# Optimization experiments

Hardware: AMD Instinct MI355X
Metric: run time of the kernel (lower is better)

Reference implementation:

```python
import jax, jax.numpy as jnp
from jax import lax
import numpy as np

RADIUS = 0.2
NSAMPLE = 32


def setup_inputs() -> dict:
    key = jax.random.key(0)
    ks = jax.random.split(key, 6)
    B, N, C = 4, 16384, 64
    xyz = jax.random.uniform(ks[0], (B, N, 3), dtype=jnp.float32)
    points = jax.random.normal(ks[1], (B, N, C), dtype=jnp.float32)
    w1 = jax.random.normal(ks[2], (64, C + 3), dtype=jnp.float32) * 0.05
    b1 = jnp.zeros((64,), jnp.float32)
    w2 = jax.random.normal(ks[3], (128, 64), dtype=jnp.float32) * 0.05
    b2 = jnp.zeros((128,), jnp.float32)
    return {"xyz": xyz, "points": points, "w1": w1, "b1": b1, "w2": w2, "b2": b2, "npoint": 1024}


def farthest_point_sampling(xyz, npoint):
    # xyz: (B,N,3). Deterministic start at index 0 (original uses a random start).
    B, N, _ = xyz.shape
    bidx = jnp.arange(B)

    def step(carry, _):
        distance, farthest = carry
        centroid = xyz[bidx, farthest]  # (B,3)
        dist = jnp.sum((xyz - centroid[:, None, :]) ** 2, axis=-1)  # (B,N)
        distance = jnp.minimum(distance, dist)
        nxt = jnp.argmax(distance, axis=-1)
        return (distance, nxt), farthest

    init = (jnp.full((B, N), 1e10, xyz.dtype), jnp.zeros((B,), jnp.int32))
    _, cents = lax.scan(step, init, None, length=npoint)  # (npoint,B)
    return cents.T  # (B,npoint)


def ball_query(xyz, new_xyz, radius, nsample):
    # xyz:(B,N,3) new_xyz:(B,S,3) -> (B,S,nsample) int indices
    N = xyz.shape[1]
    sqrdists = jnp.sum((new_xyz[:, :, None, :] - xyz[:, None, :, :]) ** 2, axis=-1)  # (B,S,N)
    idx = jnp.where(sqrdists > radius ** 2, N, jnp.arange(N))
    idx = jnp.sort(idx, axis=-1)[:, :, :nsample]
    first = idx[:, :, :1]
    return jnp.where(idx == N, first, idx)


def index_points(points, idx):
    # points:(B,N,C) idx:(B,...) -> (B,...,C)
    return jax.vmap(lambda p, i: p[i])(points, idx)


def reference(xyz, points, w1, b1, w2, b2, npoint):
    centroids = farthest_point_sampling(xyz, npoint)  # (B,S)
    new_xyz = index_points(xyz, centroids)  # (B,S,3)
    group_idx = ball_query(xyz, new_xyz, RADIUS, NSAMPLE)  # (B,S,K)
    grouped_xyz = index_points(xyz, group_idx)  # (B,S,K,3)
    grouped_xyz_norm = grouped_xyz - new_xyz[:, :, None, :]
    grouped_points = index_points(points, group_idx)  # (B,S,K,C)
    feats = jnp.concatenate([grouped_xyz_norm, grouped_points], axis=-1)  # (B,S,K,C+3)
    h = jax.nn.relu(jnp.einsum('bskc,oc->bsko', feats, w1) + b1)
    h = jax.nn.relu(jnp.einsum('bskc,oc->bsko', h, w2) + b2)  # (B,S,K,out)
    new_points = jnp.max(h, axis=2)  # (B,S,out)
    return (new_xyz, new_points)
```

## Files before the change

kernel.cpp:

```cpp
#include <hip/hip_runtime.h>

#define BB 4
#define NN 16384
#define CC 64
#define NPOINT 1024
#define NSAMPLE 32

#define FPS_T 1024
#define NCHUNK 256
#define NCELL 4096

#define REPEAT16(M) M(0) M(1) M(2) M(3) M(4) M(5) M(6) M(7) \
                    M(8) M(9) M(10) M(11) M(12) M(13) M(14) M(15)

__global__ __launch_bounds__(FPS_T) void fps_kernel(const float* __restrict__ xyz,
                                                    float* __restrict__ new_xyz,
                                                    float4* __restrict__ sorted) {
    #pragma clang fp contract(off)
    extern __shared__ char smem_raw[];
    float2* sxy  = (float2*)smem_raw;
    int*    hist = (int*)(smem_raw + 131072);
    float*  outc = (float*)(smem_raw + 131072);
    float*  lox  = (float*)(smem_raw + 147456);
    float*  loy  = lox + 272;
    float*  loz  = loy + 272;
    float*  hix  = loz + 272;
    float*  hiy  = hix + 272;
    float*  hiz  = hiy + 272;
    float4* wbc  = (float4*)(smem_raw + 153984);
    unsigned long long* slot = (unsigned long long*)(smem_raw + 154496);
    int*    wsum = (int*)(smem_raw + 154528);

    const int b    = blockIdx.x;
    const int tid  = threadIdx.x;
    const int lane = tid & 63;
    const int wv   = tid >> 6;
    const float* bx = xyz + (size_t)b * NN * 3;
    float4* sb = sorted + (size_t)b * NN;

    #pragma unroll
    for (int j = 0; j < 4; ++j) hist[j * FPS_T + tid] = 0;
    __syncthreads();

    #pragma unroll
    for (int j = 0; j < 16; ++j) {
        const int p = j * FPS_T + tid;
        const float x = bx[p * 3 + 0], y = bx[p * 3 + 1], z = bx[p * 3 + 2];
        int cx = (int)(x * 16.0f); cx = cx > 15 ? 15 : (cx < 0 ? 0 : cx);
        int cy = (int)(y * 16.0f); cy = cy > 15 ? 15 : (cy < 0 ? 0 : cy);
        int cz = (int)(z * 16.0f); cz = cz > 15 ? 15 : (cz < 0 ? 0 : cz);
        int code = 0;
        #pragma unroll
        for (int i = 0; i < 4; ++i)
            code |= (((cx >> i) & 1) << (3 * i)) |
                    (((cy >> i) & 1) << (3 * i + 1)) |
                    (((cz >> i) & 1) << (3 * i + 2));
        atomicAdd(&hist[code], 1);
    }
    __syncthreads();

    {
        const int h0 = hist[4 * tid + 0], h1 = hist[4 * tid + 1];
        const int h2 = hist[4 * tid + 2], h3 = hist[4 * tid + 3];
        const int s  = h0 + h1 + h2 + h3;
        int v = s;
        #pragma unroll
        for (int o = 1; o < 64; o <<= 1) {
            const int u = __shfl_up(v, o, 64);
            if (lane >= o) v += u;
        }
        if (lane == 63) wsum[wv] = v;
        __syncthreads();
        int base = 0;
        for (int w = 0; w < wv; ++w) base += wsum[w];
        const int e0 = base + v - s;
        hist[4 * tid + 0] = e0;
        hist[4 * tid + 1] = e0 + h0;
        hist[4 * tid + 2] = e0 + h0 + h1;
        hist[4 * tid + 3] = e0 + h0 + h1 + h2;
    }
    __syncthreads();

    #pragma unroll
    for (int j = 0; j < 16; ++j) {
        const int p = j * FPS_T + tid;
        const float x = bx[p * 3 + 0], y = bx[p * 3 + 1], z = bx[p * 3 + 2];
        int cx = (int)(x * 16.0f); cx = cx > 15 ? 15 : (cx < 0 ? 0 : cx);
        int cy = (int)(y * 16.0f); cy = cy > 15 ? 15 : (cy < 0 ? 0 : cy);
        int cz = (int)(z * 16.0f); cz = cz > 15 ? 15 : (cz < 0 ? 0 : cz);
        int code = 0;
        #pragma unroll
        for (int i = 0; i < 4; ++i)
            code |= (((cx >> i) & 1) << (3 * i)) |
                    (((cy >> i) & 1) << (3 * i + 1)) |
                    (((cz >> i) & 1) << (3 * i + 2));
        const int slotg = atomicAdd(&hist[code], 1);
        sb[slotg]  = make_float4(x, y, z, __int_as_float(p));
        sxy[slotg] = make_float2(x, y);
    }
    __syncthreads();

#define DECLZ(k) float z##k; unsigned long long key##k;
    REPEAT16(DECLZ)
#undef DECLZ
    float abx0 = 0.f, aby0 = 0.f, abz0 = 0.f, abx1 = 0.f, aby1 = 0.f, abz1 = 0.f;

#define AABBPRE(k) { const int g = wv + ((k) << 4);                       \
    const float4 pt = sb[(g << 6) + lane];                                \
    z##k = pt.z;                                                          \
    key##k = (((unsigned long long)__float_as_uint(1e10f)) << 32) |       \
             ((unsigned long long)(0x3FFFu -                              \
                    (unsigned)__float_as_int(pt.w)) << 4);                \
    float mnx = pt.x, mxx = pt.x, mny = pt.y, mxy = pt.y,                 \
          mnz = pt.z, mxz = pt.z;                                         \
    _Pragma("unroll")                                                     \
    for (int m = 32; m >= 1; m >>= 1) {                                   \
        mnx = fminf(mnx, __shfl_xor(mnx, m, 64));                         \
        mxx = fmaxf(mxx, __shfl_xor(mxx, m, 64));                         \
        mny = fminf(mny, __shfl_xor(mny, m, 64));                         \
        mxy = fmaxf(mxy, __shfl_xor(mxy, m, 64));                         \
        mnz = fminf(mnz, __shfl_xor(mnz, m, 64));                         \
        mxz = fmaxf(mxz, __shfl_xor(mxz, m, 64));                         \
    }                                                                     \
    if (lane == (k)) { abx0 = mnx; abx1 = mxx; aby0 = mny; aby1 = mxy;    \
                       abz0 = mnz; abz1 = mxz; } }
    REPEAT16(AABBPRE)
#undef AABBPRE
    if (tid == 0) { slot[0] = 0ull; slot[1] = 0ull; slot[2] = 0ull; slot[3] = 0ull; }
    __syncthreads();

    unsigned long long bkey = 0ull;
    int bestk = 0;
    int holder_ln = 0;
    float hx = 0.f, hy = 0.f, hz = 0.f;
    float cub = 1e10f;

    float ccx = bx[0], ccy = bx[1], ccz = bx[2];
    float prev_wd = 1e10f;

    for (int it = 0; it < NPOINT; ++it) {
        asm volatile("" : "+v"(z0), "+v"(z1), "+v"(z2),  "+v"(z3),
                          "+v"(z4), "+v"(z5), "+v"(z6),  "+v"(z7),
                          "+v"(z8), "+v"(z9), "+v"(z10), "+v"(z11),
                          "+v"(z12), "+v"(z13), "+v"(z14), "+v"(z15));

        if (tid == 0) {
            outc[it * 3 + 0] = ccx;
            outc[it * 3 + 1] = ccy;
            outc[it * 3 + 2] = ccz;
        }

        bool active = false;
        if (lane < 16) {
            const float dxl = fmaxf(fmaxf(abx0 - ccx, ccx - abx1), 0.0f);
            const float dyl = fmaxf(fmaxf(aby0 - ccy, ccy - aby1), 0.0f);
            const float dzl = fmaxf(fmaxf(abz0 - ccz, ccz - abz1), 0.0f);
            const float mind2 = dxl * dxl + dyl * dyl + dzl * dzl;
            const float bound = fminf(prev_wd, cub);
            active = !(mind2 > bound * 1.001f);
            if (active) {
                const float dxm = fmaxf(ccx - abx0, abx1 - ccx);
                const float dym = fmaxf(ccy - aby0, aby1 - ccy);
                const float dzm = fmaxf(ccz - abz0, abz1 - ccz);
                const float maxd2 = dxm * dxm + dym * dym + dzm * dzm;
                cub = fminf(cub, maxd2);
            }
        }
        const unsigned amask = (unsigned)(__ballot(active) & 0xFFFFull);

        bool lredo = false;
#define UPD(k) if (amask & (1u << (k))) {                                 \
            const int g = wv + ((k) << 4);                                \
            const float2 xy = sxy[(g << 6) + lane];                       \
            const float dx = xy.x - ccx;                                  \
            const float dy = xy.y - ccy;                                  \
            const float dz = z##k - ccz;                                  \
            const float t  = (dx * dx + dy * dy) + dz * dz;               \
            const float dold = __uint_as_float((unsigned)(key##k >> 32)); \
            if (t < dold) {                                               \
                key##k = (((unsigned long long)__float_as_uint(t)) << 32) \
                         | (key##k & 0xFFFFFFFFull);                      \
                lredo |= ((k) == bestk);                                  \
            }                                                             \
        }
        if (amask & 0x000Fu) { UPD(0)  UPD(1)  UPD(2)  UPD(3)  }
        if (amask & 0x00F0u) { UPD(4)  UPD(5)  UPD(6)  UPD(7)  }
        if (amask & 0x0F00u) { UPD(8)  UPD(9)  UPD(10) UPD(11) }
        if (amask & 0xF000u) { UPD(12) UPD(13) UPD(14) UPD(15) }
#undef UPD

        if (lredo) {
            bkey = 0ull; bestk = 0;
#define LM(k) if (key##k > bkey) { bkey = key##k; bestk = (k); }
            REPEAT16(LM)
#undef LM
        }

        const unsigned long long rb = __ballot(lredo);
        if ((rb >> holder_ln) & 1ull) {
            unsigned long long m = bkey;
            #pragma unroll
            for (int s = 32; s >= 1; s >>= 1) {
                const unsigned long long o = __shfl_xor(m, s, 64);
                m = o > m ? o : m;
            }
            holder_ln = __ffsll((long long)__ballot(bkey == m)) - 1;
            if (lane == holder_ln) {
                const float2 xy = sxy[((wv + (bestk << 4)) << 6) + lane];
                float zz = z0;
#define ZS(k) zz = (bestk == (k)) ? z##k : zz;
                REPEAT16(ZS)
#undef ZS
                hx = xy.x; hy = xy.y; hz = zz;
            }
        }

        if (lane == holder_ln) {
            wbc[(it & 1) * 16 + wv] = make_float4(hx, hy, hz, 0.0f);
            atomicMax(&slot[it & 3], bkey | (unsigned long long)wv);
        }
        if (tid == 0) slot[(it + 1) & 3] = 0ull;
        __syncthreads();

        const unsigned long long wk = slot[it & 3];
        prev_wd = __uint_as_float((unsigned)(wk >> 32));
        const int wwv = (int)(wk & 0xFull);
        const float4 wf = wbc[(it & 1) * 16 + wwv];
        ccx = wf.x; ccy = wf.y; ccz = wf.z;
    }

    __syncthreads();
    float* outb = new_xyz + (size_t)b * NPOINT * 3;
    #pragma unroll
    for (int j = 0; j < 3; ++j) {
        const int idx = j * FPS_T + tid;
        outb[idx] = outc[idx];
    }
}

__global__ __launch_bounds__(256) void ballq_kernel(const float* __restrict__ xyz,
                                                    const float* __restrict__ new_xyz,
                                                    int* __restrict__ gidx) {
    #pragma clang fp contract(off)
    const int lane = threadIdx.x & 63;
    const int q    = blockIdx.x * 4 + (threadIdx.x >> 6);
    const int b    = q >> 10;
    const float* bx = xyz + (size_t)b * NN * 3;
    const float* nx = new_xyz + (size_t)q * 3;
    const float cx = nx[0], cy = nx[1], cz = nx[2];
    const float rad2 = 0.04f;

    int* out  = gidx + (size_t)q * NSAMPLE;
    int taken = 0;
    int first = NN - 1;

    for (int chunk = 0; chunk < NN / 64 && taken < NSAMPLE; ++chunk) {
        const int   i  = chunk * 64 + lane;
        const float dx = cx - bx[i * 3 + 0];
        const float dy = cy - bx[i * 3 + 1];
        const float dz = cz - bx[i * 3 + 2];
        const float t  = dx * dx + dy * dy + dz * dz;
        const bool ok  = !(t > rad2);
        const unsigned long long m = __ballot(ok);
        const int cnt = __popcll(m);
        if (taken == 0 && cnt > 0) first = chunk * 64 + (__ffsll((long long)m) - 1);
        if (ok) {
            const int rank = taken + __popcll(m & ((1ull << lane) - 1ull));
            if (rank < NSAMPLE) out[rank] = i;
        }
        taken += cnt;
    }
    const int sat = taken < NSAMPLE ? taken : NSAMPLE;
    if (lane >= sat && lane < NSAMPLE) out[lane] = (taken > 0) ? first : (NN - 1);
}

__global__ __launch_bounds__(256) void mlp_kernel(const float* __restrict__ xyz,
                                                  const float* __restrict__ points,
                                                  const float* __restrict__ w1,
                                                  const float* __restrict__ b1,
                                                  const float* __restrict__ w2,
                                                  const float* __restrict__ b2,
                                                  const float* __restrict__ new_xyz,
                                                  const int*   __restrict__ gidx,
                                                  float* __restrict__ new_points) {
    __shared__ __align__(16) float feats[32][68];
    __shared__ __align__(16) float h1s[32][64];
    __shared__ float pmax[2][128];

    const int q = blockIdx.x;
    const int b = q >> 10;
    const int t = threadIdx.x;

    {
        const int k  = t >> 3;
        const int l8 = t & 7;
        const int gi = gidx[q * 32 + k];
        const float* prow = points + ((size_t)b * NN + gi) * CC;
        const float4 v0 = *(const float4*)(prow + l8 * 8);
        const float4 v1 = *(const float4*)(prow + l8 * 8 + 4);
        *(float4*)&feats[k][4 + l8 * 8] = v0;
        *(float4*)&feats[k][8 + l8 * 8] = v1;
        if (l8 == 0) {
            const float* pr = xyz + ((size_t)b * NN + gi) * 3;
            const float* nr = new_xyz + (size_t)q * 3;
            feats[k][0] = pr[0] - nr[0];
            feats[k][1] = pr[1] - nr[1];
            feats[k][2] = pr[2] - nr[2];
        }
    }

    const int c1 = t & 63;
    float w1r[67];
    #pragma unroll
    for (int j = 0; j < 67; ++j) w1r[j] = w1[c1 * 67 + j];
    const float bb1 = b1[c1];
    __syncthreads();

    const int kg = t >> 6;
    #pragma unroll
    for (int kk = 0; kk < 8; ++kk) {
        const int kr = kg * 8 + kk;
        float acc = bb1;
        acc += feats[kr][0] * w1r[0] + feats[kr][1] * w1r[1] + feats[kr][2] * w1r[2];
        #pragma unroll
        for (int j = 0; j < 64; j += 4) {
            const float4 f = *(const float4*)&feats[kr][4 + j];
            acc += f.x * w1r[3 + j] + f.y * w1r[4 + j] + f.z * w1r[5 + j] + f.w * w1r[6 + j];
        }
        h1s[kr][c1] = fmaxf(acc, 0.0f);
    }

    const int o2 = t & 127;
    const int kh = t >> 7;
    float w2r[64];
    #pragma unroll
    for (int j = 0; j < 64; ++j) w2r[j] = w2[o2 * 64 + j];
    const float bb2 = b2[o2];
    __syncthreads();

    float mx = -INFINITY;
    #pragma unroll
    for (int kk = 0; kk < 16; ++kk) {
        const int kr = kh * 16 + kk;
        float acc = bb2;
        #pragma unroll
        for (int j = 0; j < 64; j += 4) {
            const float4 h = *(const float4*)&h1s[kr][j];
            acc += h.x * w2r[j] + h.y * w2r[j + 1] + h.z * w2r[j + 2] + h.w * w2r[j + 3];
        }
        mx = fmaxf(mx, fmaxf(acc, 0.0f));
    }
    pmax[kh][o2] = mx;
    __syncthreads();
    if (t < 128) {
        new_points[(size_t)q * 128 + t] = fmaxf(pmax[0][t], pmax[1][t]);
    }
}

extern "C" void kernel_launch(void* const* d_in, const int* in_sizes, int n_in,
                              void* d_out, int out_size, void* d_ws, size_t ws_size,
                              hipStream_t stream) {
    const float* xyz    = (const float*)d_in[0];
    const float* points = (const float*)d_in[1];
    const float* w1     = (const float*)d_in[2];
    const float* b1     = (const float*)d_in[3];
    const float* w2     = (const float*)d_in[4];
    const float* b2     = (const float*)d_in[5];

    float* out_newxyz    = (float*)d_out;
    float* out_newpoints = (float*)d_out + (size_t)BB * NPOINT * 3;
    int*    gidx    = (int*)d_ws;
    float4* sortbuf = (float4*)((char*)d_ws + (size_t)512 * 1024);

    const int fps_lds = 154816;
    (void)hipFuncSetAttribute((const void*)fps_kernel,
                              hipFuncAttributeMaxDynamicSharedMemorySize,
                              fps_lds);

    fps_kernel<<<BB, FPS_T, fps_lds, stream>>>(xyz, out_newxyz, sortbuf);
    ballq_kernel<<<(BB * NPOINT) / 4, 256, 0, stream>>>(xyz, out_newxyz, gidx);
    mlp_kernel<<<BB * NPOINT, 256, 0, stream>>>(xyz, points, w1, b1, w2, b2,
                                                out_newxyz, gidx, out_newpoints);
}
```

Baseline: 1.588 ms.

## Keep FPS point coordinates and distances in registers instead of packed keys

```diff
diff --git a/kernel.cpp b/kernel.cpp
--- a/kernel.cpp
+++ b/kernel.cpp
@@ -100,17 +100,16 @@
     }
     __syncthreads();
 
-#define DECLZ(k) float z##k; unsigned long long key##k;
-    REPEAT16(DECLZ)
-#undef DECLZ
+#define DECLP(k) float x##k, y##k, z##k, d##k; unsigned tb##k;
+    REPEAT16(DECLP)
+#undef DECLP
     float abx0 = 0.f, aby0 = 0.f, abz0 = 0.f, abx1 = 0.f, aby1 = 0.f, abz1 = 0.f;
 
 #define AABBPRE(k) { const int g = wv + ((k) << 4);                       \
     const float4 pt = sb[(g << 6) + lane];                                \
-    z##k = pt.z;                                                          \
-    key##k = (((unsigned long long)__float_as_uint(1e10f)) << 32) |       \
-             ((unsigned long long)(0x3FFFu -                              \
-                    (unsigned)__float_as_int(pt.w)) << 4);                \
+    x##k = pt.x; y##k = pt.y; z##k = pt.z;                                \
+    tb##k = 0x3FFFu - (unsigned)__float_as_int(pt.w);                     \
+    d##k = 1e10f;                                                         \
     float mnx = pt.x, mxx = pt.x, mny = pt.y, mxy = pt.y,                 \
           mnz = pt.z, mxz = pt.z;                                         \
     _Pragma("unroll")                                                     \
@@ -129,9 +128,11 @@
     if (tid == 0) { slot[0] = 0ull; slot[1] = 0ull; slot[2] = 0ull; slot[3] = 0ull; }
     __syncthreads();
 
-    unsigned long long bkey = 0ull;
+    float bd = 0.0f;
+    unsigned btb = 0u;
     int bestk = 0;
     int holder_ln = 0;
+    unsigned long long hkey = 0ull;
     float hx = 0.f, hy = 0.f, hz = 0.f;
     float cub = 1e10f;
 
@@ -139,6 +140,14 @@
     float prev_wd = 1e10f;
 
     for (int it = 0; it < NPOINT; ++it) {
+        asm volatile("" : "+v"(x0), "+v"(x1), "+v"(x2),  "+v"(x3),
+                          "+v"(x4), "+v"(x5), "+v"(x6),  "+v"(x7),
+                          "+v"(x8), "+v"(x9), "+v"(x10), "+v"(x11),
+                          "+v"(x12), "+v"(x13), "+v"(x14), "+v"(x15));
+        asm volatile("" : "+v"(y0), "+v"(y1), "+v"(y2),  "+v"(y3),
+                          "+v"(y4), "+v"(y5), "+v"(y6),  "+v"(y7),
+                          "+v"(y8), "+v"(y9), "+v"(y10), "+v"(y11),
+                          "+v"(y12), "+v"(y13), "+v"(y14), "+v"(y15));
         asm volatile("" : "+v"(z0), "+v"(z1), "+v"(z2),  "+v"(z3),
                           "+v"(z4), "+v"(z5), "+v"(z6),  "+v"(z7),
                           "+v"(z8), "+v"(z9), "+v"(z10), "+v"(z11),
@@ -170,16 +179,12 @@
 
         bool lredo = false;
 #define UPD(k) if (amask & (1u << (k))) {                                 \
-            const int g = wv + ((k) << 4);                                \
-            const float2 xy = sxy[(g << 6) + lane];                       \
-            const float dx = xy.x - ccx;                                  \
-            const float dy = xy.y - ccy;                                  \
+            const float dx = x##k - ccx;                                  \
+            const float dy = y##k - ccy;                                  \
             const float dz = z##k - ccz;                                  \
             const float t  = (dx * dx + dy * dy) + dz * dz;               \
-            const float dold = __uint_as_float((unsigned)(key##k >> 32)); \
-            if (t < dold) {                                               \
-                key##k = (((unsigned long long)__float_as_uint(t)) << 32) \
-                         | (key##k & 0xFFFFFFFFull);                      \
+            if (t < d##k) {                                               \
+                d##k = t;                                                 \
                 lredo |= ((k) == bestk);                                  \
             }                                                             \
         }
@@ -190,21 +195,26 @@
 #undef UPD
 
         if (lredo) {
-            bkey = 0ull; bestk = 0;
-#define LM(k) if (key##k > bkey) { bkey = key##k; bestk = (k); }
+            bd = 0.0f; btb = 0u; bestk = 0;
+#define LM(k) if (d##k > bd || (d##k == bd && tb##k > btb)) {             \
+                  bd = d##k; btb = tb##k; bestk = (k); }
             REPEAT16(LM)
 #undef LM
         }
 
         const unsigned long long rb = __ballot(lredo);
         if ((rb >> holder_ln) & 1ull) {
-            unsigned long long m = bkey;
+            const unsigned long long bkeyv =
+                (((unsigned long long)__float_as_uint(bd)) << 32) |
+                ((unsigned long long)btb << 4);
+            unsigned long long m = bkeyv;
             #pragma unroll
             for (int s = 32; s >= 1; s >>= 1) {
                 const unsigned long long o = __shfl_xor(m, s, 64);
                 m = o > m ? o : m;
             }
-            holder_ln = __ffsll((long long)__ballot(bkey == m)) - 1;
+            holder_ln = __ffsll((long long)__ballot(bkeyv == m)) - 1;
+            hkey = m;
             if (lane == holder_ln) {
                 const float2 xy = sxy[((wv + (bestk << 4)) << 6) + lane];
                 float zz = z0;
@@ -217,16 +227,22 @@
 
         if (lane == holder_ln) {
             wbc[(it & 1) * 16 + wv] = make_float4(hx, hy, hz, 0.0f);
-            atomicMax(&slot[it & 3], bkey | (unsigned long long)wv);
+            atomicMax(&slot[it & 3], hkey | (unsigned long long)wv);
         }
         if (tid == 0) slot[(it + 1) & 3] = 0ull;
         __syncthreads();
 
         const unsigned long long wk = slot[it & 3];
+        float cwx = 0.f, cwy = 0.f, cwz = 0.f;
+        if (lane < 16) {
+            const float4 wf = wbc[(it & 1) * 16 + lane];
+            cwx = wf.x; cwy = wf.y; cwz = wf.z;
+        }
         prev_wd = __uint_as_float((unsigned)(wk >> 32));
         const int wwv = (int)(wk & 0xFull);
-        const float4 wf = wbc[(it & 1) * 16 + wwv];
-        ccx = wf.x; ccy = wf.y; ccz = wf.z;
+        ccx = __shfl(cwx, wwv, 64);
+        ccy = __shfl(cwy, wwv, 64);
+        ccz = __shfl(cwz, wwv, 64);
     }
 
     __syncthreads();
```

Result: slower. 2.128 ms (+34.0%).
